# Kernel tuning notes

Measured on AMD Instinct MI355X. Metric: run time of the kernel, lower is better.

The kernel has to match this reference:

```python
import jax, jax.numpy as jnp
import numpy as np

A = 5.0  # smoothness parameter


def setup_inputs() -> dict:
    key = jax.random.key(0)
    kx, kw = jax.random.split(key)
    x = jax.random.uniform(kx, (4096, 256), dtype=jnp.float32)
    weight = jax.random.uniform(kw, (256, 256), dtype=jnp.float32)
    return {"x": x, "weight": weight}


def reference(x, weight):
    # inner: [batch, in_features, out_features] broadcast elementwise max
    inner = jnp.maximum(x[..., None], weight[None])
    # smooth min over in_features (dim=-2): -(1/a) * logsumexp(-a * inner)
    smooth = -jax.nn.logsumexp(-A * inner, axis=-2) / A
    # hard min over same dim
    hard = jnp.min(inner, axis=-2)
    # straight-through estimator: forward value = hard, gradient flows via smooth
    return jax.lax.stop_gradient(hard - smooth) + smooth
```

## Files before the change

### kernel.cpp

```cpp
#include <hip/hip_runtime.h>


typedef _Float16 h2 __attribute__((ext_vector_type(2)));

union U4H { uint4 u; h2 h[4]; };
union U2H { uint2 u; h2 h[2]; };

static __device__ __forceinline__ h2 pmin(h2 a, h2 b) {
#if __has_builtin(__builtin_elementwise_min)
    return __builtin_elementwise_min(a, b);
#else
    h2 d; asm("v_pk_min_f16 %0, %1, %2" : "=v"(d) : "v"(a), "v"(b)); return d;
#endif
}
static __device__ __forceinline__ h2 pmax(h2 a, h2 b) {
#if __has_builtin(__builtin_elementwise_max)
    return __builtin_elementwise_max(a, b);
#else
    h2 d; asm("v_pk_max_f16 %0, %1, %2" : "=v"(d) : "v"(a), "v"(b)); return d;
#endif
}

__global__ __launch_bounds__(1024, 4)
void SmoothSTEMinMax_kernel(const float* __restrict__ x,
                            const float* __restrict__ w,
                            float* __restrict__ out) {
    __shared__ __align__(16) unsigned char smem[65536];
    unsigned char* xs = smem;
    unsigned char* ws = smem + 32768;

    const int t  = threadIdx.x;
    const int r0 = blockIdx.y * 64;
    const int c0 = blockIdx.x * 64;

    {
        const int i4 = t & 63;
        const int wv = t >> 6;
#pragma unroll
        for (int k = 0; k < 2; ++k) {
            const int rr = (k << 4) + wv;
            const float4 va = *reinterpret_cast<const float4*>(&x[(size_t)(r0 + rr)      * 256 + (i4 << 2)]);
            const float4 vb = *reinterpret_cast<const float4*>(&x[(size_t)(r0 + rr + 32) * 256 + (i4 << 2)]);
            U4H q;
            q.h[0] = h2{(_Float16)va.x, (_Float16)va.y};
            q.h[1] = h2{(_Float16)va.z, (_Float16)va.w};
            q.h[2] = h2{(_Float16)vb.x, (_Float16)vb.y};
            q.h[3] = h2{(_Float16)vb.z, (_Float16)vb.w};
            const int line = rr ^ (i4 & 31);
            *reinterpret_cast<uint4*>(xs + (i4 << 9) + (line << 4)) = q.u;
        }
    }

#pragma unroll
    for (int k = 0; k < 4; ++k) {
        const int flat = (k << 10) + t;
        const int i4  = (flat >> 6) & 63;
        const int col = flat & 63;
        const float f0 = w[(size_t)((i4 << 2) + 0) * 256 + c0 + col];
        const float f1 = w[(size_t)((i4 << 2) + 1) * 256 + c0 + col];
        const float f2 = w[(size_t)((i4 << 2) + 2) * 256 + c0 + col];
        const float f3 = w[(size_t)((i4 << 2) + 3) * 256 + c0 + col];
        U2H q;
        q.h[0] = h2{(_Float16)f0, (_Float16)f1};
        q.h[1] = h2{(_Float16)f2, (_Float16)f3};
        *reinterpret_cast<uint2*>(ws + (i4 << 9) + (col << 3)) = q.u;
    }

    __syncthreads();

    const int tr = t >> 6;
    const int tc = t & 63;

    h2 acc0, acc1, acc2, acc3;
    const h2 big = h2{(_Float16)65504.0f, (_Float16)65504.0f};
    acc0 = acc1 = acc2 = acc3 = big;

#pragma unroll 4
    for (int i4 = 0; i4 < 64; ++i4) {
        const unsigned char* xb = xs + (i4 << 9);
        const int kk = i4 & 31;
        U4H xu0, xu1; U2H wq;
        xu0.u = *reinterpret_cast<const uint4*>(xb + ((((tr << 1)    ) ^ kk) << 4));
        xu1.u = *reinterpret_cast<const uint4*>(xb + ((((tr << 1) | 1) ^ kk) << 4));
        wq.u  = *reinterpret_cast<const uint2*>(ws + (i4 << 9) + (tc << 3));

        const h2 wA = wq.h[0], wB = wq.h[1];
        acc0 = pmin(acc0, pmax(xu0.h[0], wA)); acc0 = pmin(acc0, pmax(xu0.h[1], wB));
        acc1 = pmin(acc1, pmax(xu0.h[2], wA)); acc1 = pmin(acc1, pmax(xu0.h[3], wB));
        acc2 = pmin(acc2, pmax(xu1.h[0], wA)); acc2 = pmin(acc2, pmax(xu1.h[1], wB));
        acc3 = pmin(acc3, pmax(xu1.h[2], wA)); acc3 = pmin(acc3, pmax(xu1.h[3], wB));
    }

    const int rowm[4] = { 2 * tr, 2 * tr + 32, 2 * tr + 1, 2 * tr + 33 };
    const float o0 = fminf((float)acc0.x, (float)acc0.y);
    const float o1 = fminf((float)acc1.x, (float)acc1.y);
    const float o2 = fminf((float)acc2.x, (float)acc2.y);
    const float o3 = fminf((float)acc3.x, (float)acc3.y);
    out[(size_t)(r0 + rowm[0]) * 256 + c0 + tc] = o0;
    out[(size_t)(r0 + rowm[1]) * 256 + c0 + tc] = o1;
    out[(size_t)(r0 + rowm[2]) * 256 + c0 + tc] = o2;
    out[(size_t)(r0 + rowm[3]) * 256 + c0 + tc] = o3;
}

extern "C" void kernel_launch(void* const* d_in, const int* in_sizes, int n_in,
                              void* d_out, int out_size, void* d_ws, size_t ws_size,
                              hipStream_t stream) {
    const float* x = (const float*)d_in[0];
    const float* w = (const float*)d_in[1];
    float* out = (float*)d_out;

    const int batch = in_sizes[0] / 256;
    dim3 grid(256 / 64, batch / 64);
    dim3 block(1024);
    hipLaunchKernelGGL(SmoothSTEMinMax_kernel, grid, block, 0, stream, x, w, out);
}
```

Measured before the change: 23.46 us.

## Split into fp16 prepack kernel and LDS-free scalar-load min-max main kernel

Adds a prepack kernel that converts x and weight to packed fp16 in the workspace, with x in a 4-row interleaved layout and weight transposed for 16-byte per-lane loads. The main kernel drops shared memory and reads x per wave through scalar s_load_dwordx16 into SGPRs, so v_pk_max takes a scalar operand. Weight is read with global_load_dwordx4 and double-buffered against the compute. This trades the LDS staging and barrier for an extra kernel launch and a round trip of the converted data through global memory.

```diff
diff --git a/kernel.cpp b/kernel.cpp
--- a/kernel.cpp
+++ b/kernel.cpp
@@ -2,104 +2,100 @@
 
 
 typedef _Float16 h2 __attribute__((ext_vector_type(2)));
-
-union U4H { uint4 u; h2 h[4]; };
-union U2H { uint2 u; h2 h[2]; };
+typedef int i16v __attribute__((ext_vector_type(16)));
 
 static __device__ __forceinline__ h2 pmin(h2 a, h2 b) {
-#if __has_builtin(__builtin_elementwise_min)
     return __builtin_elementwise_min(a, b);
-#else
-    h2 d; asm("v_pk_min_f16 %0, %1, %2" : "=v"(d) : "v"(a), "v"(b)); return d;
-#endif
-}
-static __device__ __forceinline__ h2 pmax(h2 a, h2 b) {
-#if __has_builtin(__builtin_elementwise_max)
-    return __builtin_elementwise_max(a, b);
-#else
-    h2 d; asm("v_pk_max_f16 %0, %1, %2" : "=v"(d) : "v"(a), "v"(b)); return d;
-#endif
 }
 
-__global__ __launch_bounds__(1024, 4)
-void SmoothSTEMinMax_kernel(const float* __restrict__ x,
-                            const float* __restrict__ w,
-                            float* __restrict__ out) {
-    __shared__ __align__(16) unsigned char smem[65536];
-    unsigned char* xs = smem;
-    unsigned char* ws = smem + 32768;
+__global__ __launch_bounds__(256)
+void prepack_kernel(const float* __restrict__ x, const float* __restrict__ w,
+                    unsigned int* __restrict__ xt, unsigned int* __restrict__ wq) {
+    const int tid = blockIdx.x * 256 + threadIdx.x;
+    if (tid < 524288) {
+        const int j  = tid & 3;
+        const int rr = (tid >> 2) & 3;
+        const int c  = (tid >> 4) & 31;
+        const int r4 = tid >> 9;
+        const int row = (r4 << 2) + rr;
+        const float2 v = *reinterpret_cast<const float2*>(&x[(size_t)row * 256 + (c << 3) + (j << 1)]);
+        const h2 p = h2{(_Float16)v.x, (_Float16)v.y};
+        xt[tid] = __builtin_bit_cast(unsigned int, p);
+    } else {
+        const int u   = tid - 524288;
+        const int col = u & 255;
+        const int j   = (u >> 8) & 3;
+        const int c   = u >> 10;
+        const int i0  = (c << 3) + (j << 1);
+        const h2 p = h2{(_Float16)w[(size_t)i0 * 256 + col], (_Float16)w[(size_t)(i0 + 1) * 256 + col]};
+        wq[(size_t)((((c << 8) + col) << 2) + j)] = __builtin_bit_cast(unsigned int, p);
+    }
+}
 
-    const int t  = threadIdx.x;
-    const int r0 = blockIdx.y * 64;
-    const int c0 = blockIdx.x * 64;
+#define PKSTEP(XS, WV, ACC) do { int _t;                                     \
+    asm("v_pk_max_f16 %0, %1, %2" : "=v"(_t) : "s"(XS), "v"(WV));            \
+    ACC = pmin(ACC, __builtin_bit_cast(h2, _t)); } while (0)
 
-    {
-        const int i4 = t & 63;
-        const int wv = t >> 6;
-#pragma unroll
-        for (int k = 0; k < 2; ++k) {
-            const int rr = (k << 4) + wv;
-            const float4 va = *reinterpret_cast<const float4*>(&x[(size_t)(r0 + rr)      * 256 + (i4 << 2)]);
-            const float4 vb = *reinterpret_cast<const float4*>(&x[(size_t)(r0 + rr + 32) * 256 + (i4 << 2)]);
-            U4H q;
-            q.h[0] = h2{(_Float16)va.x, (_Float16)va.y};
-            q.h[1] = h2{(_Float16)va.z, (_Float16)va.w};
-            q.h[2] = h2{(_Float16)vb.x, (_Float16)vb.y};
-            q.h[3] = h2{(_Float16)vb.z, (_Float16)vb.w};
-            const int line = rr ^ (i4 & 31);
-            *reinterpret_cast<uint4*>(xs + (i4 << 9) + (line << 4)) = q.u;
-        }
+#define STEP16(Xv, Wv) do {                                                                                  \
+    PKSTEP(Xv[0],  Wv.x, acc0); PKSTEP(Xv[1],  Wv.y, acc0); PKSTEP(Xv[2],  Wv.z, acc0); PKSTEP(Xv[3],  Wv.w, acc0); \
+    PKSTEP(Xv[4],  Wv.x, acc1); PKSTEP(Xv[5],  Wv.y, acc1); PKSTEP(Xv[6],  Wv.z, acc1); PKSTEP(Xv[7],  Wv.w, acc1); \
+    PKSTEP(Xv[8],  Wv.x, acc2); PKSTEP(Xv[9],  Wv.y, acc2); PKSTEP(Xv[10], Wv.z, acc2); PKSTEP(Xv[11], Wv.w, acc2); \
+    PKSTEP(Xv[12], Wv.x, acc3); PKSTEP(Xv[13], Wv.y, acc3); PKSTEP(Xv[14], Wv.z, acc3); PKSTEP(Xv[15], Wv.w, acc3); \
+} while (0)
+
+#define WAITALL() do {                                                       \
+    asm volatile("s_waitcnt lgkmcnt(0) vmcnt(0)" ::: "memory");              \
+    __builtin_amdgcn_sched_barrier(0); } while (0)
+
+#define PF_X(DST, ADDR) asm volatile("s_load_dwordx16 %0, %1, 0x0" : "=s"(DST) : "s"(ADDR))
+#define PF_W(DST, OFF)  asm volatile("global_load_dwordx4 %0, %1, %2" : "=v"(DST) : "v"(OFF), "s"(wb))
+
+__global__ __launch_bounds__(256, 4)
+void stemm_main(const unsigned int* __restrict__ xt, const unsigned int* __restrict__ wq,
+                float* __restrict__ out) {
+    const int t    = threadIdx.x;
+    const int lane = t & 63;
+    const int wv   = __builtin_amdgcn_readfirstlane(t >> 6);
+    const int c0   = (blockIdx.x & 3) << 6;
+    const int rb   = blockIdx.x >> 2;
+    const int r4   = (rb << 2) + wv;
+
+    unsigned long long xa = (unsigned long long)xt + ((unsigned long long)r4 << 11);
+    unsigned int       wo = (unsigned int)((c0 + lane) << 4);
+    const unsigned long long wb = (unsigned long long)wq;
+
+    i16v X0{}, X1{};
+    uint4 W0{0, 0, 0, 0}, W1{0, 0, 0, 0};
+
+    PF_X(X0, xa); PF_W(W0, wo);
+    unsigned long long xan = xa + 64;
+    unsigned int       won = wo + 4096;
+
+    h2 acc0 = h2{(_Float16)65504.0f, (_Float16)65504.0f};
+    h2 acc1 = acc0, acc2 = acc0, acc3 = acc0;
+
+#pragma unroll 1
+    for (int cc = 0; cc < 15; ++cc) {
+        WAITALL();
+        PF_X(X1, xan); PF_W(W1, won);
+        xan += 64; won += 4096;
+        STEP16(X0, W0);
+        WAITALL();
+        PF_X(X0, xan); PF_W(W0, won);
+        xan += 64; won += 4096;
+        STEP16(X1, W1);
     }
+    WAITALL();
+    PF_X(X1, xan); PF_W(W1, won);
+    STEP16(X0, W0);
+    WAITALL();
+    STEP16(X1, W1);
 
-#pragma unroll
-    for (int k = 0; k < 4; ++k) {
-        const int flat = (k << 10) + t;
-        const int i4  = (flat >> 6) & 63;
-        const int col = flat & 63;
-        const float f0 = w[(size_t)((i4 << 2) + 0) * 256 + c0 + col];
-        const float f1 = w[(size_t)((i4 << 2) + 1) * 256 + c0 + col];
-        const float f2 = w[(size_t)((i4 << 2) + 2) * 256 + c0 + col];
-        const float f3 = w[(size_t)((i4 << 2) + 3) * 256 + c0 + col];
-        U2H q;
-        q.h[0] = h2{(_Float16)f0, (_Float16)f1};
-        q.h[1] = h2{(_Float16)f2, (_Float16)f3};
-        *reinterpret_cast<uint2*>(ws + (i4 << 9) + (col << 3)) = q.u;
-    }
-
-    __syncthreads();
-
-    const int tr = t >> 6;
-    const int tc = t & 63;
-
-    h2 acc0, acc1, acc2, acc3;
-    const h2 big = h2{(_Float16)65504.0f, (_Float16)65504.0f};
-    acc0 = acc1 = acc2 = acc3 = big;
-
-#pragma unroll 4
-    for (int i4 = 0; i4 < 64; ++i4) {
-        const unsigned char* xb = xs + (i4 << 9);
-        const int kk = i4 & 31;
-        U4H xu0, xu1; U2H wq;
-        xu0.u = *reinterpret_cast<const uint4*>(xb + ((((tr << 1)    ) ^ kk) << 4));
-        xu1.u = *reinterpret_cast<const uint4*>(xb + ((((tr << 1) | 1) ^ kk) << 4));
-        wq.u  = *reinterpret_cast<const uint2*>(ws + (i4 << 9) + (tc << 3));
-
-        const h2 wA = wq.h[0], wB = wq.h[1];
-        acc0 = pmin(acc0, pmax(xu0.h[0], wA)); acc0 = pmin(acc0, pmax(xu0.h[1], wB));
-        acc1 = pmin(acc1, pmax(xu0.h[2], wA)); acc1 = pmin(acc1, pmax(xu0.h[3], wB));
-        acc2 = pmin(acc2, pmax(xu1.h[0], wA)); acc2 = pmin(acc2, pmax(xu1.h[1], wB));
-        acc3 = pmin(acc3, pmax(xu1.h[2], wA)); acc3 = pmin(acc3, pmax(xu1.h[3], wB));
-    }
-
-    const int rowm[4] = { 2 * tr, 2 * tr + 32, 2 * tr + 1, 2 * tr + 33 };
-    const float o0 = fminf((float)acc0.x, (float)acc0.y);
-    const float o1 = fminf((float)acc1.x, (float)acc1.y);
-    const float o2 = fminf((float)acc2.x, (float)acc2.y);
-    const float o3 = fminf((float)acc3.x, (float)acc3.y);
-    out[(size_t)(r0 + rowm[0]) * 256 + c0 + tc] = o0;
-    out[(size_t)(r0 + rowm[1]) * 256 + c0 + tc] = o1;
-    out[(size_t)(r0 + rowm[2]) * 256 + c0 + tc] = o2;
-    out[(size_t)(r0 + rowm[3]) * 256 + c0 + tc] = o3;
+    const int r0 = r4 << 2;
+    out[(size_t)(r0 + 0) * 256 + c0 + lane] = fminf((float)acc0.x, (float)acc0.y);
+    out[(size_t)(r0 + 1) * 256 + c0 + lane] = fminf((float)acc1.x, (float)acc1.y);
+    out[(size_t)(r0 + 2) * 256 + c0 + lane] = fminf((float)acc2.x, (float)acc2.y);
+    out[(size_t)(r0 + 3) * 256 + c0 + lane] = fminf((float)acc3.x, (float)acc3.y);
 }
 
 extern "C" void kernel_launch(void* const* d_in, const int* in_sizes, int n_in,
@@ -109,8 +105,9 @@
     const float* w = (const float*)d_in[1];
     float* out = (float*)d_out;
 
-    const int batch = in_sizes[0] / 256;
-    dim3 grid(256 / 64, batch / 64);
-    dim3 block(1024);
-    hipLaunchKernelGGL(SmoothSTEMinMax_kernel, grid, block, 0, stream, x, w, out);
+    unsigned int* xt = (unsigned int*)d_ws;
+    unsigned int* wq = (unsigned int*)((char*)d_ws + (2u << 20));
+
+    hipLaunchKernelGGL(prepack_kernel, dim3(2176), dim3(256), 0, stream, x, w, xt, wq);
+    hipLaunchKernelGGL(stemm_main, dim3(1024), dim3(256), 0, stream, xt, wq, out);
 }
```

Result: slower. 26.25 us (+11.9%).
